# Performance work log

Measured on AMD Instinct MI355X. Metric: run time of the kernel, lower is better.

Reference implementation:

```python
import jax, jax.numpy as jnp
import numpy as np

N_HEADS = 16


def setup_inputs() -> dict:
    key = jax.random.key(0)
    k1, k2, k3, k4 = jax.random.split(key, 4)
    b, s, d = 2, 2048, 1024
    x = jax.random.normal(k1, (b, s, d), dtype=jnp.float32)
    attn_B = jax.random.normal(k2, (b, N_HEADS, s, s), dtype=jnp.float32) * 0.02
    W_attn = jax.random.normal(k3, (d, 3 * d), dtype=jnp.float32) * (1.0 / np.sqrt(d))
    b_attn = jax.random.normal(k4, (3 * d,), dtype=jnp.float32) * 0.01
    return {"x": x, "attn_B": attn_B, "W_attn": W_attn, "b_attn": b_attn}


def reference(x, attn_B, W_attn, b_attn):
    b, s, d = x.shape
    h = N_HEADS
    hd = d // h
    qkv = x @ W_attn + b_attn                       # [b, s, 3d]
    Q, K, V = jnp.split(qkv, 3, axis=-1)
    # [b, s, d] -> [b, h, s, hd]
    Q = Q.reshape(b, s, h, hd).transpose(0, 2, 1, 3)
    K = K.reshape(b, s, h, hd).transpose(0, 2, 1, 3)
    V = V.reshape(b, s, h, hd).transpose(0, 2, 1, 3)
    scale = 1.0 / jnp.sqrt(jnp.asarray(hd, dtype=Q.dtype))
    scores = jnp.einsum("bhqk,bhsk->bhqs", Q, K) * scale   # [b, h, s, s]
    attn = jax.nn.softmax(scores, axis=-1) + attn_B          # post-softmax additive bias
    y = jnp.einsum("bhqs,bhsd->bhqd", attn, V)               # [b, h, s, hd]
    y = y.transpose(0, 2, 1, 3).reshape(b, s, d)
    return y
```

## Files before the change

kernel.cpp:

```cpp
#include <hip/hip_runtime.h>
#include <hip/hip_bf16.h>


typedef __attribute__((ext_vector_type(4))) float  f32x4;
typedef __attribute__((ext_vector_type(8))) short  bf16x8;
typedef __attribute__((ext_vector_type(4))) short  s16x4;

__device__ inline short f2bf(float f) {
    __hip_bfloat16 h = __float2bfloat16(f);
    return __builtin_bit_cast(short, h);
}

__global__ void conv_x_kernel(const float* __restrict__ x, short* __restrict__ xb) {
    int idx = blockIdx.x * 256 + threadIdx.x;
    f32x4 v = *reinterpret_cast<const f32x4*>(x + (size_t)idx * 4);
    s16x4 o;
    o[0] = f2bf(v[0]); o[1] = f2bf(v[1]); o[2] = f2bf(v[2]); o[3] = f2bf(v[3]);
    *reinterpret_cast<s16x4*>(xb + (size_t)idx * 4) = o;
}

__global__ void wtrans_kernel(const float* __restrict__ W, short* __restrict__ Wt) {
    __shared__ float tile[64][65];
    int kb = blockIdx.x;
    int nb = blockIdx.y;
    int t = threadIdx.x;
    int c4 = (t & 15) * 4;
    int r0 = t >> 4;
#pragma unroll
    for (int rr = 0; rr < 4; ++rr) {
        int kl = r0 + rr * 16;
        f32x4 v = *reinterpret_cast<const f32x4*>(W + (size_t)(kb * 64 + kl) * 3072 + nb * 64 + c4);
        tile[kl][c4 + 0] = v[0]; tile[kl][c4 + 1] = v[1];
        tile[kl][c4 + 2] = v[2]; tile[kl][c4 + 3] = v[3];
    }
    __syncthreads();
#pragma unroll
    for (int rr = 0; rr < 4; ++rr) {
        int nl = r0 + rr * 16;
        s16x4 o;
#pragma unroll
        for (int i = 0; i < 4; ++i) o[i] = f2bf(tile[c4 + i][nl]);
        *reinterpret_cast<s16x4*>(Wt + (size_t)(nb * 64 + nl) * 1024 + kb * 64 + c4) = o;
    }
}

__global__ __launch_bounds__(256) void qkv_gemm_kernel(
    const short* __restrict__ xb, const short* __restrict__ Wt,
    const float* __restrict__ bias,
    short* __restrict__ Qo, short* __restrict__ Ko, short* __restrict__ Vo)
{
    __shared__ short As[128 * 64];
    __shared__ short Bs[128 * 64];
    int tid = threadIdx.x;
    int wave = tid >> 6, lane = tid & 63, g = lane >> 4, lr = lane & 15;
    int wr = wave >> 1, wc = wave & 1;
    int bm = blockIdx.x, bn = blockIdx.y;

    f32x4 acc[4][4];
#pragma unroll
    for (int a = 0; a < 4; ++a)
#pragma unroll
        for (int b = 0; b < 4; ++b) acc[a][b] = (f32x4){0.f, 0.f, 0.f, 0.f};

    for (int k0 = 0; k0 < 1024; k0 += 64) {
#pragma unroll
        for (int j = 0; j < 4; ++j) {
            int c = tid + 256 * j;
            int row = c >> 3, cc = c & 7;
            bf16x8 va = *reinterpret_cast<const bf16x8*>(xb + (size_t)(bm * 128 + row) * 1024 + k0 + cc * 8);
            *reinterpret_cast<bf16x8*>(&As[row * 64 + ((cc ^ (row & 7)) * 8)]) = va;
            bf16x8 vb = *reinterpret_cast<const bf16x8*>(Wt + (size_t)(bn * 128 + row) * 1024 + k0 + cc * 8);
            *reinterpret_cast<bf16x8*>(&Bs[row * 64 + ((cc ^ (row & 7)) * 8)]) = vb;
        }
        __syncthreads();

        bf16x8 af[2][4], bfr[2][4];
#pragma unroll
        for (int mt = 0; mt < 4; ++mt) {
            int row = wr * 64 + mt * 16 + lr;
            af[0][mt] = *reinterpret_cast<const bf16x8*>(&As[row * 64 + (((g    ) ^ (lr & 7)) * 8)]);
            af[1][mt] = *reinterpret_cast<const bf16x8*>(&As[row * 64 + (((g + 4) ^ (lr & 7)) * 8)]);
        }
#pragma unroll
        for (int nt = 0; nt < 4; ++nt) {
            int row = wc * 64 + nt * 16 + lr;
            bfr[0][nt] = *reinterpret_cast<const bf16x8*>(&Bs[row * 64 + (((g    ) ^ (lr & 7)) * 8)]);
            bfr[1][nt] = *reinterpret_cast<const bf16x8*>(&Bs[row * 64 + (((g + 4) ^ (lr & 7)) * 8)]);
        }
#pragma unroll
        for (int mt = 0; mt < 4; ++mt)
#pragma unroll
            for (int nt = 0; nt < 4; ++nt) {
                acc[mt][nt] = __builtin_amdgcn_mfma_f32_16x16x32_bf16(af[0][mt], bfr[0][nt], acc[mt][nt], 0, 0, 0);
                acc[mt][nt] = __builtin_amdgcn_mfma_f32_16x16x32_bf16(af[1][mt], bfr[1][nt], acc[mt][nt], 0, 0, 0);
            }
        __syncthreads();
    }

#pragma unroll
    for (int nt = 0; nt < 4; ++nt) {
        int n = bn * 128 + wc * 64 + nt * 16 + lr;
        float bv = bias[n];
        int which = n >> 10;
        int h = (n >> 6) & 15;
        int dd = n & 63;
        short* base = (which == 0) ? Qo : (which == 1) ? Ko : Vo;
#pragma unroll
        for (int mt = 0; mt < 4; ++mt) {
#pragma unroll
            for (int r = 0; r < 4; ++r) {
                int m = bm * 128 + wr * 64 + mt * 16 + g * 4 + r;
                int bb = m >> 11, s = m & 2047;
                float v = acc[mt][nt][r] + bv;
                base[(((size_t)bb * 16 + h) * 2048 + s) * 64 + dd] = f2bf(v);
            }
        }
    }
}

__global__ __launch_bounds__(256) void attn_kernel(
    const short* __restrict__ Qw, const short* __restrict__ Kw, const short* __restrict__ Vw,
    const float* __restrict__ attnB, float* __restrict__ out)
{
    __shared__ short Ks [64][64];
    __shared__ short Vts[64][64];
    __shared__ short Ps [4][16][64];

    int qt = blockIdx.x;
    int bh = blockIdx.y;
    int b = bh >> 4, h = bh & 15;
    int tid = threadIdx.x;
    int wave = tid >> 6, lane = tid & 63, g = lane >> 4, lr = lane & 15;

    const short* Qbase = Qw + (size_t)bh * 2048 * 64;
    const short* Kbase = Kw + (size_t)bh * 2048 * 64;
    const short* Vbase = Vw + (size_t)bh * 2048 * 64;
    const float* Bbase = attnB + (size_t)bh * 2048 * 2048;

    int qbase = qt * 64 + wave * 16;

    bf16x8 qf[2];
    {
        const short* qp = Qbase + (size_t)(qbase + lr) * 64 + g * 8;
        qf[0] = *reinterpret_cast<const bf16x8*>(qp);
        qf[1] = *reinterpret_cast<const bf16x8*>(qp + 32);
    }

    f32x4 Os[4], Ob[4];
#pragma unroll
    for (int dt = 0; dt < 4; ++dt) { Os[dt] = (f32x4){0.f,0.f,0.f,0.f}; Ob[dt] = (f32x4){0.f,0.f,0.f,0.f}; }
    float mrun[4], lrun[4];
#pragma unroll
    for (int r = 0; r < 4; ++r) { mrun[r] = -1e30f; lrun[r] = 0.f; }

    for (int kt = 0; kt < 32; ++kt) {
#pragma unroll
        for (int j = 0; j < 2; ++j) {
            int c = tid + 256 * j;
            int row = c >> 3, cc = c & 7;
            bf16x8 v = *reinterpret_cast<const bf16x8*>(Kbase + (size_t)(kt * 64 + row) * 64 + cc * 8);
            *reinterpret_cast<bf16x8*>(&Ks[row][(cc ^ (row & 7)) * 8]) = v;
        }
#pragma unroll
        for (int j = 0; j < 2; ++j) {
            int c = tid + 256 * j;
            int key = c & 63, cc = c >> 6;
            bf16x8 v = *reinterpret_cast<const bf16x8*>(Vbase + (size_t)(kt * 64 + key) * 64 + cc * 8);
#pragma unroll
            for (int i = 0; i < 8; ++i) {
                int d = cc * 8 + i;
                Vts[d][(((key >> 3) ^ (d & 7)) * 8) + (key & 7)] = v[i];
            }
        }
        __syncthreads();

        f32x4 bfl[4];
        {
            const float* bp = Bbase + (size_t)(qbase + lr) * 2048 + kt * 64 + g * 8;
            bfl[0] = *reinterpret_cast<const f32x4*>(bp);
            bfl[1] = *reinterpret_cast<const f32x4*>(bp + 4);
            bfl[2] = *reinterpret_cast<const f32x4*>(bp + 32);
            bfl[3] = *reinterpret_cast<const f32x4*>(bp + 36);
        }

        f32x4 S[4];
#pragma unroll
        for (int nt = 0; nt < 4; ++nt) {
            int krow = nt * 16 + lr;
            bf16x8 kf0 = *reinterpret_cast<const bf16x8*>(&Ks[krow][(((g    ) ^ (lr & 7)) * 8)]);
            bf16x8 kf1 = *reinterpret_cast<const bf16x8*>(&Ks[krow][(((g + 4) ^ (lr & 7)) * 8)]);
            f32x4 s = (f32x4){0.f,0.f,0.f,0.f};
            s = __builtin_amdgcn_mfma_f32_16x16x32_bf16(qf[0], kf0, s, 0, 0, 0);
            s = __builtin_amdgcn_mfma_f32_16x16x32_bf16(qf[1], kf1, s, 0, 0, 0);
            S[nt] = s;
        }

#pragma unroll
        for (int nt = 0; nt < 4; ++nt)
#pragma unroll
            for (int r = 0; r < 4; ++r) S[nt][r] *= 0.125f;

#pragma unroll
        for (int r = 0; r < 4; ++r) {
            float mx = fmaxf(fmaxf(S[0][r], S[1][r]), fmaxf(S[2][r], S[3][r]));
            mx = fmaxf(mx, __shfl_xor(mx, 1));
            mx = fmaxf(mx, __shfl_xor(mx, 2));
            mx = fmaxf(mx, __shfl_xor(mx, 4));
            mx = fmaxf(mx, __shfl_xor(mx, 8));
            float newm = fmaxf(mrun[r], mx);
            float sf = __expf(mrun[r] - newm);
            mrun[r] = newm;
            float rs = 0.f;
#pragma unroll
            for (int nt = 0; nt < 4; ++nt) {
                float p = __expf(S[nt][r] - newm);
                S[nt][r] = p;
                rs += p;
            }
            rs += __shfl_xor(rs, 1);
            rs += __shfl_xor(rs, 2);
            rs += __shfl_xor(rs, 4);
            rs += __shfl_xor(rs, 8);
            lrun[r] = lrun[r] * sf + rs;
#pragma unroll
            for (int dt = 0; dt < 4; ++dt) Os[dt][r] *= sf;
        }

#pragma unroll
        for (int nt = 0; nt < 4; ++nt) {
#pragma unroll
            for (int r = 0; r < 4; ++r) {
                int q = g * 4 + r;
                int col = nt * 16 + lr;
                Ps[wave][q][(((col >> 3) ^ (q & 7)) * 8) + (col & 7)] = f2bf(S[nt][r]);
            }
        }

        bf16x8 bbf[2];
#pragma unroll
        for (int i = 0; i < 4; ++i) {
            bbf[0][i]     = f2bf(bfl[0][i]);
            bbf[0][i + 4] = f2bf(bfl[1][i]);
            bbf[1][i]     = f2bf(bfl[2][i]);
            bbf[1][i + 4] = f2bf(bfl[3][i]);
        }

        bf16x8 pf0 = *reinterpret_cast<const bf16x8*>(&Ps[wave][lr][(((g    ) ^ (lr & 7)) * 8)]);
        bf16x8 pf1 = *reinterpret_cast<const bf16x8*>(&Ps[wave][lr][(((g + 4) ^ (lr & 7)) * 8)]);
#pragma unroll
        for (int dt = 0; dt < 4; ++dt) {
            int vrow = dt * 16 + lr;
            bf16x8 v0 = *reinterpret_cast<const bf16x8*>(&Vts[vrow][(((g    ) ^ (lr & 7)) * 8)]);
            bf16x8 v1 = *reinterpret_cast<const bf16x8*>(&Vts[vrow][(((g + 4) ^ (lr & 7)) * 8)]);
            Os[dt] = __builtin_amdgcn_mfma_f32_16x16x32_bf16(pf0,    v0, Os[dt], 0, 0, 0);
            Os[dt] = __builtin_amdgcn_mfma_f32_16x16x32_bf16(pf1,    v1, Os[dt], 0, 0, 0);
            Ob[dt] = __builtin_amdgcn_mfma_f32_16x16x32_bf16(bbf[0], v0, Ob[dt], 0, 0, 0);
            Ob[dt] = __builtin_amdgcn_mfma_f32_16x16x32_bf16(bbf[1], v1, Ob[dt], 0, 0, 0);
        }
        __syncthreads();
    }

#pragma unroll
    for (int dt = 0; dt < 4; ++dt) {
#pragma unroll
        for (int r = 0; r < 4; ++r) {
            int q = qbase + g * 4 + r;
            int dcol = dt * 16 + lr;
            float v = Os[dt][r] / lrun[r] + Ob[dt][r];
            out[((size_t)(b * 2048 + q) * 16 + h) * 64 + dcol] = v;
        }
    }
}

extern "C" void kernel_launch(void* const* d_in, const int* in_sizes, int n_in,
                              void* d_out, int out_size, void* d_ws, size_t ws_size,
                              hipStream_t stream) {
    const float* x     = (const float*)d_in[0];
    const float* attnB = (const float*)d_in[1];
    const float* W     = (const float*)d_in[2];
    const float* bias  = (const float*)d_in[3];
    float* out = (float*)d_out;

    short* ws = (short*)d_ws;
    short* xb = ws;
    short* Wt = xb + 4194304;
    short* Q  = Wt + 3145728;
    short* K  = Q  + 4194304;
    short* V  = K  + 4194304;

    conv_x_kernel<<<4096, 256, 0, stream>>>(x, xb);
    wtrans_kernel<<<dim3(16, 48), 256, 0, stream>>>(W, Wt);
    qkv_gemm_kernel<<<dim3(32, 24), 256, 0, stream>>>(xb, Wt, bias, Q, K, V);
    attn_kernel<<<dim3(32, 32), 256, 0, stream>>>(Q, K, V, attnB, out);
}
```

Before: 245.4 us.

## Double-buffer K/V via direct global-to-LDS loads, pre-transpose V, drop online max

```diff
diff --git a/kernel.cpp b/kernel.cpp
--- a/kernel.cpp
+++ b/kernel.cpp
@@ -6,9 +6,15 @@
 typedef __attribute__((ext_vector_type(8))) short  bf16x8;
 typedef __attribute__((ext_vector_type(4))) short  s16x4;
 
-__device__ inline short f2bf(float f) {
+__device__ __forceinline__ short f2bf(float f) {
     __hip_bfloat16 h = __float2bfloat16(f);
     return __builtin_bit_cast(short, h);
+}
+
+__device__ __forceinline__ void gll16(const short* g, short* l) {
+    __builtin_amdgcn_global_load_lds(
+        (const __attribute__((address_space(1))) void*)g,
+        (__attribute__((address_space(3))) void*)l, 16, 0, 0);
 }
 
 __global__ void conv_x_kernel(const float* __restrict__ x, short* __restrict__ xb) {
@@ -21,8 +27,7 @@
 
 __global__ void wtrans_kernel(const float* __restrict__ W, short* __restrict__ Wt) {
     __shared__ float tile[64][65];
-    int kb = blockIdx.x;
-    int nb = blockIdx.y;
+    int kb = blockIdx.x, nb = blockIdx.y;
     int t = threadIdx.x;
     int c4 = (t & 15) * 4;
     int r0 = t >> 4;
@@ -65,12 +70,13 @@
     for (int k0 = 0; k0 < 1024; k0 += 64) {
 #pragma unroll
         for (int j = 0; j < 4; ++j) {
-            int c = tid + 256 * j;
+            int c = j * 256 + tid;
             int row = c >> 3, cc = c & 7;
-            bf16x8 va = *reinterpret_cast<const bf16x8*>(xb + (size_t)(bm * 128 + row) * 1024 + k0 + cc * 8);
-            *reinterpret_cast<bf16x8*>(&As[row * 64 + ((cc ^ (row & 7)) * 8)]) = va;
-            bf16x8 vb = *reinterpret_cast<const bf16x8*>(Wt + (size_t)(bn * 128 + row) * 1024 + k0 + cc * 8);
-            *reinterpret_cast<bf16x8*>(&Bs[row * 64 + ((cc ^ (row & 7)) * 8)]) = vb;
+            int scc = (cc ^ (row & 7)) * 8;
+            gll16(xb + (size_t)(bm * 128 + row) * 1024 + k0 + scc,
+                  &As[(j * 256 + wave * 64) * 8]);
+            gll16(Wt + (size_t)(bn * 128 + row) * 1024 + k0 + scc,
+                  &Bs[(j * 256 + wave * 64) * 8]);
         }
         __syncthreads();
 
@@ -118,156 +124,161 @@
     }
 }
 
+__global__ __launch_bounds__(256) void vtrans_kernel(const short* __restrict__ V, short* __restrict__ Vt) {
+    __shared__ short t[64][72];
+    int st = blockIdx.x, bh = blockIdx.y;
+    int tid = threadIdx.x;
+#pragma unroll
+    for (int j = 0; j < 2; ++j) {
+        int c = j * 256 + tid;
+        int row = c >> 3, cc = c & 7;
+        bf16x8 v = *reinterpret_cast<const bf16x8*>(V + (size_t)((bh * 2048) + st * 64 + row) * 64 + cc * 8);
+        *reinterpret_cast<bf16x8*>(&t[row][cc * 8]) = v;
+    }
+    __syncthreads();
+#pragma unroll
+    for (int j = 0; j < 2; ++j) {
+        int c = j * 256 + tid;
+        int d = c >> 3, cs = c & 7;
+        bf16x8 o;
+#pragma unroll
+        for (int i = 0; i < 8; ++i) o[i] = t[cs * 8 + i][d];
+        *reinterpret_cast<bf16x8*>(Vt + (size_t)(bh * 64 + d) * 2048 + st * 64 + cs * 8) = o;
+    }
+}
+
 __global__ __launch_bounds__(256) void attn_kernel(
-    const short* __restrict__ Qw, const short* __restrict__ Kw, const short* __restrict__ Vw,
+    const short* __restrict__ Qw, const short* __restrict__ Kw, const short* __restrict__ Vtw,
     const float* __restrict__ attnB, float* __restrict__ out)
 {
-    __shared__ short Ks [64][64];
-    __shared__ short Vts[64][64];
-    __shared__ short Ps [4][16][64];
-
-    int qt = blockIdx.x;
-    int bh = blockIdx.y;
+    __shared__ short Ks [2][64 * 64];
+    __shared__ short Vts[2][64 * 64];
+    __shared__ short Ps [4][16 * 64];
+
+    int qt = blockIdx.x, bh = blockIdx.y;
     int b = bh >> 4, h = bh & 15;
     int tid = threadIdx.x;
     int wave = tid >> 6, lane = tid & 63, g = lane >> 4, lr = lane & 15;
 
-    const short* Qbase = Qw + (size_t)bh * 2048 * 64;
-    const short* Kbase = Kw + (size_t)bh * 2048 * 64;
-    const short* Vbase = Vw + (size_t)bh * 2048 * 64;
-    const float* Bbase = attnB + (size_t)bh * 2048 * 2048;
+    const short* Qb = Qw  + (size_t)bh * 2048 * 64;
+    const short* Kb = Kw  + (size_t)bh * 2048 * 64;
+    const short* Vb = Vtw + (size_t)bh * 64 * 2048;
+    const float* Bp = attnB + (size_t)bh * 2048 * 2048;
 
     int qbase = qt * 64 + wave * 16;
 
-    bf16x8 qf[2];
+    bf16x8 qf0, qf1;
     {
-        const short* qp = Qbase + (size_t)(qbase + lr) * 64 + g * 8;
-        qf[0] = *reinterpret_cast<const bf16x8*>(qp);
-        qf[1] = *reinterpret_cast<const bf16x8*>(qp + 32);
-    }
+        const short* qp = Qb + (size_t)(qbase + lr) * 64 + g * 8;
+        qf0 = *reinterpret_cast<const bf16x8*>(qp);
+        qf1 = *reinterpret_cast<const bf16x8*>(qp + 32);
+    }
+    const float* brow = Bp + (size_t)(qbase + lr) * 2048 + g * 8;
 
     f32x4 Os[4], Ob[4];
 #pragma unroll
     for (int dt = 0; dt < 4; ++dt) { Os[dt] = (f32x4){0.f,0.f,0.f,0.f}; Ob[dt] = (f32x4){0.f,0.f,0.f,0.f}; }
-    float mrun[4], lrun[4];
-#pragma unroll
-    for (int r = 0; r < 4; ++r) { mrun[r] = -1e30f; lrun[r] = 0.f; }
+    float lpart[4] = {0.f, 0.f, 0.f, 0.f};
+
+#define STAGE_KV(buf, ktt) do {                                                   \
+    _Pragma("unroll")                                                             \
+    for (int j = 0; j < 2; ++j) {                                                 \
+        int c = j * 256 + tid;                                                    \
+        int row = c >> 3, cc = c & 7;                                             \
+        int scc = (cc ^ (row & 7)) * 8;                                           \
+        gll16(Kb + (size_t)((ktt) * 64 + row) * 64 + scc,                         \
+              &Ks[buf][(j * 256 + wave * 64) * 8]);                               \
+        gll16(Vb + (size_t)row * 2048 + (ktt) * 64 + scc,                         \
+              &Vts[buf][(j * 256 + wave * 64) * 8]);                              \
+    }                                                                             \
+} while (0)
+
+    STAGE_KV(0, 0);
+    __syncthreads();
 
     for (int kt = 0; kt < 32; ++kt) {
-#pragma unroll
-        for (int j = 0; j < 2; ++j) {
-            int c = tid + 256 * j;
-            int row = c >> 3, cc = c & 7;
-            bf16x8 v = *reinterpret_cast<const bf16x8*>(Kbase + (size_t)(kt * 64 + row) * 64 + cc * 8);
-            *reinterpret_cast<bf16x8*>(&Ks[row][(cc ^ (row & 7)) * 8]) = v;
-        }
-#pragma unroll
-        for (int j = 0; j < 2; ++j) {
-            int c = tid + 256 * j;
-            int key = c & 63, cc = c >> 6;
-            bf16x8 v = *reinterpret_cast<const bf16x8*>(Vbase + (size_t)(kt * 64 + key) * 64 + cc * 8);
-#pragma unroll
-            for (int i = 0; i < 8; ++i) {
-                int d = cc * 8 + i;
-                Vts[d][(((key >> 3) ^ (d & 7)) * 8) + (key & 7)] = v[i];
+        int cur = kt & 1;
+        if (kt < 31) STAGE_KV(cur ^ 1, kt + 1);
+
+        f32x4 bfl0 = *reinterpret_cast<const f32x4*>(brow + kt * 64);
+        f32x4 bfl1 = *reinterpret_cast<const f32x4*>(brow + kt * 64 + 4);
+        f32x4 bfl2 = *reinterpret_cast<const f32x4*>(brow + kt * 64 + 32);
+        f32x4 bfl3 = *reinterpret_cast<const f32x4*>(brow + kt * 64 + 36);
+
+        f32x4 S[4];
+        __builtin_amdgcn_s_setprio(1);
+#pragma unroll
+        for (int nt = 0; nt < 4; ++nt) {
+            int row = nt * 16 + lr;
+            bf16x8 kf0 = *reinterpret_cast<const bf16x8*>(&Ks[cur][row * 64 + (((g    ) ^ (lr & 7)) * 8)]);
+            bf16x8 kf1 = *reinterpret_cast<const bf16x8*>(&Ks[cur][row * 64 + (((g + 4) ^ (lr & 7)) * 8)]);
+            f32x4 s = (f32x4){0.f,0.f,0.f,0.f};
+            s = __builtin_amdgcn_mfma_f32_16x16x32_bf16(qf0, kf0, s, 0, 0, 0);
+            s = __builtin_amdgcn_mfma_f32_16x16x32_bf16(qf1, kf1, s, 0, 0, 0);
+            S[nt] = s;
+        }
+        __builtin_amdgcn_s_setprio(0);
+
+#pragma unroll
+        for (int nt = 0; nt < 4; ++nt)
+#pragma unroll
+            for (int r = 0; r < 4; ++r) {
+                float p = __expf(S[nt][r] * 0.125f);
+                S[nt][r] = p;
+                lpart[r] += p;
             }
-        }
-        __syncthreads();
-
-        f32x4 bfl[4];
-        {
-            const float* bp = Bbase + (size_t)(qbase + lr) * 2048 + kt * 64 + g * 8;
-            bfl[0] = *reinterpret_cast<const f32x4*>(bp);
-            bfl[1] = *reinterpret_cast<const f32x4*>(bp + 4);
-            bfl[2] = *reinterpret_cast<const f32x4*>(bp + 32);
-            bfl[3] = *reinterpret_cast<const f32x4*>(bp + 36);
-        }
-
-        f32x4 S[4];
-#pragma unroll
-        for (int nt = 0; nt < 4; ++nt) {
-            int krow = nt * 16 + lr;
-            bf16x8 kf0 = *reinterpret_cast<const bf16x8*>(&Ks[krow][(((g    ) ^ (lr & 7)) * 8)]);
-            bf16x8 kf1 = *reinterpret_cast<const bf16x8*>(&Ks[krow][(((g + 4) ^ (lr & 7)) * 8)]);
-            f32x4 s = (f32x4){0.f,0.f,0.f,0.f};
-            s = __builtin_amdgcn_mfma_f32_16x16x32_bf16(qf[0], kf0, s, 0, 0, 0);
-            s = __builtin_amdgcn_mfma_f32_16x16x32_bf16(qf[1], kf1, s, 0, 0, 0);
-            S[nt] = s;
-        }
 
 #pragma unroll
         for (int nt = 0; nt < 4; ++nt)
-#pragma unroll
-            for (int r = 0; r < 4; ++r) S[nt][r] *= 0.125f;
-
-#pragma unroll
-        for (int r = 0; r < 4; ++r) {
-            float mx = fmaxf(fmaxf(S[0][r], S[1][r]), fmaxf(S[2][r], S[3][r]));
-            mx = fmaxf(mx, __shfl_xor(mx, 1));
-            mx = fmaxf(mx, __shfl_xor(mx, 2));
-            mx = fmaxf(mx, __shfl_xor(mx, 4));
-            mx = fmaxf(mx, __shfl_xor(mx, 8));
-            float newm = fmaxf(mrun[r], mx);
-            float sf = __expf(mrun[r] - newm);
-            mrun[r] = newm;
-            float rs = 0.f;
-#pragma unroll
-            for (int nt = 0; nt < 4; ++nt) {
-                float p = __expf(S[nt][r] - newm);
-                S[nt][r] = p;
-                rs += p;
-            }
-            rs += __shfl_xor(rs, 1);
-            rs += __shfl_xor(rs, 2);
-            rs += __shfl_xor(rs, 4);
-            rs += __shfl_xor(rs, 8);
-            lrun[r] = lrun[r] * sf + rs;
-#pragma unroll
-            for (int dt = 0; dt < 4; ++dt) Os[dt][r] *= sf;
-        }
-
-#pragma unroll
-        for (int nt = 0; nt < 4; ++nt) {
 #pragma unroll
             for (int r = 0; r < 4; ++r) {
                 int q = g * 4 + r;
                 int col = nt * 16 + lr;
-                Ps[wave][q][(((col >> 3) ^ (q & 7)) * 8) + (col & 7)] = f2bf(S[nt][r]);
+                Ps[wave][q * 64 + (((col >> 3) ^ (q & 7)) * 8) + (col & 7)] = f2bf(S[nt][r]);
             }
-        }
-
-        bf16x8 bbf[2];
+
+        bf16x8 bbf0, bbf1;
 #pragma unroll
         for (int i = 0; i < 4; ++i) {
-            bbf[0][i]     = f2bf(bfl[0][i]);
-            bbf[0][i + 4] = f2bf(bfl[1][i]);
-            bbf[1][i]     = f2bf(bfl[2][i]);
-            bbf[1][i + 4] = f2bf(bfl[3][i]);
-        }
-
-        bf16x8 pf0 = *reinterpret_cast<const bf16x8*>(&Ps[wave][lr][(((g    ) ^ (lr & 7)) * 8)]);
-        bf16x8 pf1 = *reinterpret_cast<const bf16x8*>(&Ps[wave][lr][(((g + 4) ^ (lr & 7)) * 8)]);
+            bbf0[i]     = f2bf(bfl0[i]);
+            bbf0[i + 4] = f2bf(bfl1[i]);
+            bbf1[i]     = f2bf(bfl2[i]);
+            bbf1[i + 4] = f2bf(bfl3[i]);
+        }
+
+        bf16x8 pf0 = *reinterpret_cast<const bf16x8*>(&Ps[wave][lr * 64 + (((g    ) ^ (lr & 7)) * 8)]);
+        bf16x8 pf1 = *reinterpret_cast<const bf16x8*>(&Ps[wave][lr * 64 + (((g + 4) ^ (lr & 7)) * 8)]);
+
+        __builtin_amdgcn_s_setprio(1);
 #pragma unroll
         for (int dt = 0; dt < 4; ++dt) {
-            int vrow = dt * 16 + lr;
-            bf16x8 v0 = *reinterpret_cast<const bf16x8*>(&Vts[vrow][(((g    ) ^ (lr & 7)) * 8)]);
-            bf16x8 v1 = *reinterpret_cast<const bf16x8*>(&Vts[vrow][(((g + 4) ^ (lr & 7)) * 8)]);
-            Os[dt] = __builtin_amdgcn_mfma_f32_16x16x32_bf16(pf0,    v0, Os[dt], 0, 0, 0);
-            Os[dt] = __builtin_amdgcn_mfma_f32_16x16x32_bf16(pf1,    v1, Os[dt], 0, 0, 0);
-            Ob[dt] = __builtin_amdgcn_mfma_f32_16x16x32_bf16(bbf[0], v0, Ob[dt], 0, 0, 0);
-            Ob[dt] = __builtin_amdgcn_mfma_f32_16x16x32_bf16(bbf[1], v1, Ob[dt], 0, 0, 0);
-        }
+            int row = dt * 16 + lr;
+            bf16x8 v0 = *reinterpret_cast<const bf16x8*>(&Vts[cur][row * 64 + (((g    ) ^ (lr & 7)) * 8)]);
+            bf16x8 v1 = *reinterpret_cast<const bf16x8*>(&Vts[cur][row * 64 + (((g + 4) ^ (lr & 7)) * 8)]);
+            Os[dt] = __builtin_amdgcn_mfma_f32_16x16x32_bf16(pf0,  v0, Os[dt], 0, 0, 0);
+            Os[dt] = __builtin_amdgcn_mfma_f32_16x16x32_bf16(pf1,  v1, Os[dt], 0, 0, 0);
+            Ob[dt] = __builtin_amdgcn_mfma_f32_16x16x32_bf16(bbf0, v0, Ob[dt], 0, 0, 0);
+            Ob[dt] = __builtin_amdgcn_mfma_f32_16x16x32_bf16(bbf1, v1, Ob[dt], 0, 0, 0);
+        }
+        __builtin_amdgcn_s_setprio(0);
+
         __syncthreads();
     }
-
-#pragma unroll
-    for (int dt = 0; dt < 4; ++dt) {
-#pragma unroll
-        for (int r = 0; r < 4; ++r) {
-            int q = qbase + g * 4 + r;
+#undef STAGE_KV
+
+#pragma unroll
+    for (int r = 0; r < 4; ++r) {
+        float l = lpart[r];
+        l += __shfl_xor(l, 1);
+        l += __shfl_xor(l, 2);
+        l += __shfl_xor(l, 4);
+        l += __shfl_xor(l, 8);
+        float inv = 1.0f / l;
+        int q = qbase + g * 4 + r;
+#pragma unroll
+        for (int dt = 0; dt < 4; ++dt) {
             int dcol = dt * 16 + lr;
-            float v = Os[dt][r] / lrun[r] + Ob[dt][r];
-            out[((size_t)(b * 2048 + q) * 16 + h) * 64 + dcol] = v;
+            out[((size_t)(b * 2048 + q) * 16 + h) * 64 + dcol] = Os[dt][r] * inv + Ob[dt][r];
         }
     }
 }
@@ -287,9 +298,11 @@
     short* Q  = Wt + 3145728;
     short* K  = Q  + 4194304;
     short* V  = K  + 4194304;
+    short* Vt = V  + 4194304;
 
     conv_x_kernel<<<4096, 256, 0, stream>>>(x, xb);
     wtrans_kernel<<<dim3(16, 48), 256, 0, stream>>>(W, Wt);
     qkv_gemm_kernel<<<dim3(32, 24), 256, 0, stream>>>(xb, Wt, bias, Q, K, V);
-    attn_kernel<<<dim3(32, 32), 256, 0, stream>>>(Q, K, V, attnB, out);
-}
+    vtrans_kernel<<<dim3(32, 32), 256, 0, stream>>>(V, Vt);
+    attn_kernel<<<dim3(32, 32), 256, 0, stream>>>(Q, K, Vt, attnB, out);
+}
```

After: 228.6 us. 6.8% less time.
